# Optimization experiments

Measured on AMD Instinct MI355X. Metric: run time of the kernel, lower is better.

The kernel has to match this reference:

```python
import jax, jax.numpy as jnp
import numpy as np

COMMITMENT_COST = 0.25
ENTROPY_WEIGHT = 0.1
EPS = 1e-10


def setup_inputs() -> dict:
    key = jax.random.key(0)
    k1, k2 = jax.random.split(key)
    B, L, D, K = 8, 4096, 256, 4096
    z = jax.random.normal(k1, (B, L, D), dtype=jnp.float32)
    # torch init: uniform(-1/K, 1/K)
    codebook_weight = jax.random.uniform(k2, (K, D), dtype=jnp.float32,
                                         minval=-1.0 / K, maxval=1.0 / K)
    return {"z": z, "codebook_weight": codebook_weight}


def reference(z, codebook_weight):
    B, L, D = z.shape
    z_flat = z.reshape(-1, D)                       # [N, D]
    # squared euclidean distances: [N, K]
    d2 = (jnp.sum(z_flat ** 2, axis=1, keepdims=True)
          + jnp.sum(codebook_weight ** 2, axis=1)
          - 2.0 * z_flat @ codebook_weight.T)
    indices = jnp.argmin(d2, axis=1)                # [N]
    z_q_flat = codebook_weight[indices]             # gather [N, D]
    z_q = z_q_flat.reshape(B, L, D)

    codebook_loss = jnp.mean((z_q - jax.lax.stop_gradient(z)) ** 2)
    commitment_loss = jnp.mean((jax.lax.stop_gradient(z_q) - z) ** 2)

    probs = jax.nn.softmax(-d2, axis=1)             # [N, K]
    avg_probs = probs.mean(axis=0)                  # [K]
    entropy = -jnp.sum(avg_probs * jnp.log(avg_probs + EPS))
    entropy_loss = -entropy

    codebook_commitment_loss = codebook_loss + COMMITMENT_COST * commitment_loss
    scaled_entropy_loss = ENTROPY_WEIGHT * entropy_loss
    vq_loss = codebook_commitment_loss + scaled_entropy_loss

    # straight-through estimator
    z_q_ste = z + jax.lax.stop_gradient(z_q - z)
    indices_out = indices.reshape(B, L)
    return (z_q_ste, indices_out, vq_loss, codebook_commitment_loss, scaled_entropy_loss)
```

## Files before the change

### kernel.cpp

```cpp
#include <hip/hip_runtime.h>
#include <stdint.h>

#define NROWS 32768
#define KC 4096
#define DIM 256
#define BM 128
#define NWV 8
#define TPS 64
#define CAP 40
#define KAPPA 0.99960f
#define K2L2E 2.88539008f
#define L2E 1.44269504f

#define OUT_IDX (NROWS * DIM)
#define OUT_SCAL (OUT_IDX + NROWS)

#define WS_CNORM 0
#define WS_ZNORM 16384
#define WS_LOSS  147456
#define WS_AVGP8 147712
#define WS_FRAG  278784

typedef __bf16 bf8 __attribute__((ext_vector_type(8)));
typedef float f16v __attribute__((ext_vector_type(16)));

#define GLOAD_LDS(g, l) \
  __builtin_amdgcn_global_load_lds( \
      (const __attribute__((address_space(1))) void*)(g), \
      (__attribute__((address_space(3))) void*)(l), 16, 0, 0)

__device__ __forceinline__ unsigned ford(float f) {
  unsigned u = __float_as_uint(f);
  return (u & 0x80000000u) ? ~u : (u | 0x80000000u);
}

__device__ __forceinline__ float np_rownorm256(const float* __restrict__ p) {
  float h[2];
  #pragma unroll
  for (int half = 0; half < 2; ++half) {
    const float* b = p + half * 128;
    float r[8];
    #pragma unroll
    for (int j = 0; j < 8; ++j) { float v = b[j]; r[j] = __fmul_rn(v, v); }
    for (int i = 8; i < 128; i += 8) {
      #pragma unroll
      for (int j = 0; j < 8; ++j) {
        float v = b[i + j];
        r[j] = __fadd_rn(r[j], __fmul_rn(v, v));
      }
    }
    h[half] = __fadd_rn(
        __fadd_rn(__fadd_rn(r[0], r[1]), __fadd_rn(r[2], r[3])),
        __fadd_rn(__fadd_rn(r[4], r[5]), __fadd_rn(r[6], r[7])));
  }
  return __fadd_rn(h[0], h[1]);
}

__global__ void k_norms(const float* __restrict__ cbw, const float* __restrict__ z,
                        float* __restrict__ cnorm, float* __restrict__ znorm) {
  int r = blockIdx.x * 256 + threadIdx.x;
  if (r < KC) cnorm[r] = np_rownorm256(cbw + (size_t)r * DIM);
  else {
    int q = r - KC;
    if (q < NROWS) znorm[q] = np_rownorm256(z + (size_t)q * DIM);
  }
}

__global__ void k_frag(const float* __restrict__ cbw, __bf16* __restrict__ frag) {
  int idx = blockIdx.x * 256 + threadIdx.x;
  int c = idx >> 5, u = idx & 31;
  int ds = u >> 1, half = u & 1;
  int ct = c >> 5, m = c & 31;
  int lane = half * 32 + m;
  const float* src = cbw + (size_t)c * DIM + ds * 16 + half * 8;
  float4 a = *(const float4*)src;
  float4 b = *(const float4*)(src + 4);
  bf8 h;
  h[0] = (__bf16)a.x; h[1] = (__bf16)a.y; h[2] = (__bf16)a.z; h[3] = (__bf16)a.w;
  h[4] = (__bf16)b.x; h[5] = (__bf16)b.y; h[6] = (__bf16)b.z; h[7] = (__bf16)b.w;
  *(bf8*)(frag + ((size_t)(ct * 16 + ds) * 64 + lane) * 8) = h;
}

__device__ __forceinline__ float exact_d2(const float* __restrict__ zr,
                                          const float* __restrict__ cr,
                                          float rn, float cn) {
  float mm = 0.f;
  for (int d = 0; d < DIM; d += 4) {
    float4 zv = *(const float4*)(zr + d);
    float4 cv = *(const float4*)(cr + d);
    mm = __builtin_fmaf(zv.x, cv.x, mm);
    mm = __builtin_fmaf(zv.y, cv.y, mm);
    mm = __builtin_fmaf(zv.z, cv.z, mm);
    mm = __builtin_fmaf(zv.w, cv.w, mm);
  }
  return __fsub_rn(__fadd_rn(rn, cn), __fmul_rn(2.f, mm));
}

#define BLD(bs, c) (*(const bf8*)((bs) + (c) * 512 + lane * 8))

#define AQ_ALL(OP) OP(0) OP(1) OP(2) OP(3) OP(4) OP(5) OP(6) OP(7) \
                   OP(8) OP(9) OP(10) OP(11) OP(12) OP(13) OP(14) OP(15)
#define AQ_DECL(i) const bf8 aq##i = \
  *(const bf8*)&Aimg[((size_t)(wr * 16 + (i)) * 64 + lane) * 8];

#define MF(A, B) acc = __builtin_amdgcn_mfma_f32_32x32x16_bf16((A), (B), acc, 0, 0, 0);
#define CONSUME_H0(bs) { MF(aq0, BLD(bs,0)) MF(aq1, BLD(bs,1)) MF(aq2, BLD(bs,2)) \
  MF(aq3, BLD(bs,3)) MF(aq4, BLD(bs,4)) MF(aq5, BLD(bs,5)) MF(aq6, BLD(bs,6)) \
  MF(aq7, BLD(bs,7)) }
#define CONSUME_H1(bs) { MF(aq8, BLD(bs,0)) MF(aq9, BLD(bs,1)) MF(aq10, BLD(bs,2)) \
  MF(aq11, BLD(bs,3)) MF(aq12, BLD(bs,4)) MF(aq13, BLD(bs,5)) MF(aq14, BLD(bs,6)) \
  MF(aq15, BLD(bs,7)) }

__global__ __launch_bounds__(512, 2) void k_main(
    const float* __restrict__ z, const float* __restrict__ cbw,
    const float* __restrict__ cnorm, const float* __restrict__ znorm,
    const __bf16* __restrict__ frag, float* __restrict__ out,
    float* __restrict__ avgp8, double* __restrict__ losssum) {
  __shared__ __attribute__((aligned(16))) __bf16 Aimg[4 * 16 * 64 * 8];
  __shared__ __attribute__((aligned(16))) __bf16 Bst[2][2][4096];
  __shared__ float cnormL[KC];
  __shared__ int cand[BM][CAP];
  __shared__ int ccount[BM];
  __shared__ unsigned rowmaxU[BM];
  __shared__ unsigned long long rowkey[BM];
  __shared__ float esumL[BM], invR[BM], lred[512];
  __shared__ int idxr[BM];

  const int t = threadIdx.x;
  const int lane = t & 63, wv = t >> 6;
  const int ln31 = lane & 31, lh = lane >> 5;
  const int wr = wv & 3, wc = wv >> 2;
  const int row0 = blockIdx.x * BM;
  const int ctbase = wc * TPS;

  if (t < BM) {
    ccount[t] = 0; rowmaxU[t] = 0u; rowkey[t] = ~0ULL; esumL[t] = 0.f;
  }

  #pragma unroll
  for (int i = 0; i < 8; ++i) cnormL[t + 512 * i] = cnorm[t + 512 * i];

  #pragma unroll
  for (int i = 0; i < 8; ++i) {
    int idx = i * 512 + t;
    int l = idx & 63, ds = (idx >> 6) & 15, rt = idx >> 10;
    int row = rt * 32 + (l & 31), d0 = ds * 16 + (l >> 5) * 8;
    const float* src = z + (size_t)(row0 + row) * DIM + d0;
    float4 a = *(const float4*)src;
    float4 b = *(const float4*)(src + 4);
    bf8 h;
    h[0] = (__bf16)a.x; h[1] = (__bf16)a.y; h[2] = (__bf16)a.z; h[3] = (__bf16)a.w;
    h[4] = (__bf16)b.x; h[5] = (__bf16)b.y; h[6] = (__bf16)b.z; h[7] = (__bf16)b.w;
    *(bf8*)&Aimg[((size_t)((rt * 16 + ds) * 64 + l)) * 8] = h;
  }
  __syncthreads();

  AQ_ALL(AQ_DECL)

  #define STAGE2(ct, h, buf) { \
    const char* g_ = (const char*)frag + (size_t)(ct) * 16384 + (size_t)(h) * 8192 \
                     + wr * 2048 + (size_t)lane * 16; \
    char* l_ = (char*)Bst + (buf) * 16384 + wc * 8192 + wr * 2048; \
    GLOAD_LDS(g_, l_); \
    GLOAD_LDS(g_ + 1024, l_ + 1024); \
  }

  float es[16];
  #pragma unroll
  for (int i = 0; i < 16; ++i) es[i] = 0.f;

  {
    STAGE2(ctbase, 0, 0)
    __syncthreads();
    for (int tt = 0; tt < 65; ++tt) {
      const int ct = ctbase + (tt ? tt - 1 : 0);
      STAGE2(ct, 1, 1)
      f16v acc;
      #pragma unroll
      for (int r = 0; r < 16; ++r) acc[r] = 0.f;
      float cr[16];
      {
        const float4* rmf = (const float4*)(rowmaxU + wr * 32);
        float4 c0 = rmf[lh], c1 = rmf[2 + lh], c2 = rmf[4 + lh], c3 = rmf[6 + lh];
        cr[0]  = c0.x; cr[1]  = c0.y; cr[2]  = c0.z; cr[3]  = c0.w;
        cr[4]  = c1.x; cr[5]  = c1.y; cr[6]  = c1.z; cr[7]  = c1.w;
        cr[8]  = c2.x; cr[9]  = c2.y; cr[10] = c2.z; cr[11] = c2.w;
        cr[12] = c3.x; cr[13] = c3.y; cr[14] = c3.z; cr[15] = c3.w;
      }
      {
        const __bf16* bs = (const __bf16*)((const char*)Bst + 0 * 16384 + wc * 8192);
        CONSUME_H0(bs)
      }
      __syncthreads();
      {
        int ctn = ctbase + ((tt < 64) ? tt : 63);
        STAGE2(ctn, 0, 0)
      }
      {
        const __bf16* bs = (const __bf16*)((const char*)Bst + 1 * 16384 + wc * 8192);
        CONSUME_H1(bs)
      }
      const float cnl = cnormL[ct * 32 + ln31] * L2E;
      if (tt == 0) {
        #pragma unroll
        for (int r = 0; r < 16; ++r) {
          const int row = wr * 32 + (r & 3) + 8 * (r >> 2) + 4 * lh;
          float e = exp2f(__builtin_fmaf(acc[r], K2L2E, -cnl));
          atomicMax(&rowmaxU[row], __float_as_uint(e));
        }
      } else {
        unsigned cond = 0u;
        #pragma unroll
        for (int r = 0; r < 16; ++r) {
          float e = exp2f(__builtin_fmaf(acc[r], K2L2E, -cnl));
          es[r] += e;
          cond |= (e >= cr[r] * KAPPA) ? (1u << r) : 0u;
        }
        if (cond) {
          #pragma unroll
          for (int r = 0; r < 16; ++r) {
            if (cond & (1u << r)) {
              const int row = wr * 32 + (r & 3) + 8 * (r >> 2) + 4 * lh;
              float e = exp2f(__builtin_fmaf(acc[r], K2L2E, -cnl));
              atomicMax(&rowmaxU[row], __float_as_uint(e));
              int slot = atomicAdd(&ccount[row], 1);
              if (slot < CAP) cand[row][slot] = ct * 32 + ln31;
            }
          }
        }
      }
      __syncthreads();
    }
  }

  #pragma unroll
  for (int r = 0; r < 16; ++r) {
    float e = es[r];
    #pragma unroll
    for (int off = 16; off > 0; off >>= 1) e += __shfl_xor(e, off);
    if (ln31 == 0) {
      const int row = wr * 32 + (r & 3) + 8 * (r >> 2) + 4 * lh;
      atomicAdd(&esumL[row], e);
    }
  }
  __syncthreads();
  if (t < BM) invR[t] = 1.0f / esumL[t];
  __syncthreads();

  {
    int r = t & 127, q = t >> 7;
    int cnt = ccount[r];
    const float* zr = z + (size_t)(row0 + r) * DIM;
    float rn = znorm[row0 + r];
    if (cnt <= CAP) {
      for (int s = q; s < cnt; s += 4) {
        int k = cand[r][s];
        float d2 = exact_d2(zr, cbw + (size_t)k * DIM, rn, cnormL[k]);
        atomicMin(&rowkey[r], (((unsigned long long)ford(d2)) << 32) | (unsigned)k);
      }
    } else {
      for (int k = q; k < KC; k += 4) {
        float d2 = exact_d2(zr, cbw + (size_t)k * DIM, rn, cnormL[k]);
        atomicMin(&rowkey[r], (((unsigned long long)ford(d2)) << 32) | (unsigned)k);
      }
    }
  }
  __syncthreads();
  if (t < BM) {
    int idx = (int)(rowkey[t] & 0xFFFFFFFFULL);
    idxr[t] = idx;
    out[OUT_IDX + row0 + t] = (float)idx;
  }
  __syncthreads();

  float lacc = 0.f;
  {
    const int col = t & 255;
    for (int r = (t >> 8); r < BM; r += 2) {
      int idx = idxr[r];
      float zq = cbw[(size_t)idx * DIM + col];
      float zv = z[(size_t)(row0 + r) * DIM + col];
      float df = __fsub_rn(zq, zv);
      out[(size_t)(row0 + r) * DIM + col] = __fadd_rn(zv, df);
      lacc += df * df;
    }
  }
  lred[t] = lacc;
  __syncthreads();
  #pragma unroll
  for (int s = 256; s > 0; s >>= 1) {
    if (t < s) lred[t] += lred[t + s];
    __syncthreads();
  }
  if (t == 0) atomicAdd(losssum, (double)lred[0]);

  float ir[16];
  #pragma unroll
  for (int r = 0; r < 16; ++r)
    ir[r] = invR[wr * 32 + (r & 3) + 8 * (r >> 2) + 4 * lh];
  __syncthreads();

  {
    float* shadow = avgp8 + (size_t)(blockIdx.x & 7) * KC;
    STAGE2(ctbase, 0, 0)
    __syncthreads();
    for (int tt = 0; tt < 64; ++tt) {
      const int ct = ctbase + tt;
      STAGE2(ct, 1, 1)
      f16v acc;
      #pragma unroll
      for (int r = 0; r < 16; ++r) acc[r] = 0.f;
      {
        const __bf16* bs = (const __bf16*)((const char*)Bst + 0 * 16384 + wc * 8192);
        CONSUME_H0(bs)
      }
      __syncthreads();
      {
        int ctn = ctbase + ((tt < 63) ? tt + 1 : 63);
        STAGE2(ctn, 0, 0)
      }
      {
        const __bf16* bs = (const __bf16*)((const char*)Bst + 1 * 16384 + wc * 8192);
        CONSUME_H1(bs)
      }
      const float cnl = cnormL[ct * 32 + ln31] * L2E;
      float s2 = 0.f;
      #pragma unroll
      for (int r = 0; r < 16; ++r) {
        float e = exp2f(__builtin_fmaf(acc[r], K2L2E, -cnl));
        s2 = __builtin_fmaf(e, ir[r], s2);
      }
      s2 += __shfl_xor(s2, 32);
      if (lh == 0) atomicAdd(&shadow[ct * 32 + ln31], s2);
      __syncthreads();
    }
  }
}

__global__ void k_final(const float* __restrict__ avgp8,
                        const double* __restrict__ losssum,
                        float* __restrict__ out) {
  const int t = threadIdx.x;
  double part = 0.0;
  for (int k = t; k < KC; k += 256) {
    float a4 = 0.f;
    #pragma unroll
    for (int s = 0; s < 8; ++s) a4 += avgp8[s * KC + k];
    double a = (double)a4 / (double)NROWS;
    part += a * log(a + 1e-10);
  }
  __shared__ double sd[256];
  sd[t] = part;
  __syncthreads();
  for (int s = 128; s > 0; s >>= 1) {
    if (t < s) sd[t] += sd[t + s];
    __syncthreads();
  }
  if (t == 0) {
    double H = -sd[0];
    double mse = losssum[0] / (double)((size_t)NROWS * DIM);
    double ccl = 1.25 * mse;
    double sel = -0.1 * H;
    out[OUT_SCAL + 0] = (float)(ccl + sel);
    out[OUT_SCAL + 1] = (float)ccl;
    out[OUT_SCAL + 2] = (float)sel;
  }
}

extern "C" void kernel_launch(void* const* d_in, const int* in_sizes, int n_in,
                              void* d_out, int out_size, void* d_ws, size_t ws_size,
                              hipStream_t stream) {
  const float* z = (const float*)d_in[0];
  const float* cbw = (const float*)d_in[1];
  float* out = (float*)d_out;
  char* ws = (char*)d_ws;
  float* cnorm = (float*)(ws + WS_CNORM);
  float* znorm = (float*)(ws + WS_ZNORM);
  double* losssum = (double*)(ws + WS_LOSS);
  float* avgp8 = (float*)(ws + WS_AVGP8);
  __bf16* frag = (__bf16*)(ws + WS_FRAG);

  hipMemsetAsync(ws + WS_LOSS, 0, 8, stream);
  hipMemsetAsync(ws + WS_AVGP8, 0, 8 * KC * 4, stream);
  k_norms<<<(KC + NROWS) / 256, 256, 0, stream>>>(cbw, z, cnorm, znorm);
  k_frag<<<(KC * 32) / 256, 256, 0, stream>>>(cbw, frag);
  k_main<<<NROWS / BM, 512, 0, stream>>>(z, cbw, cnorm, znorm, frag, out,
                                         avgp8, losssum);
  k_final<<<1, 256, 0, stream>>>(avgp8, losssum, out);
}
```

Measured before the change: 454.2 us.

## Shrink row block to 64 and alias A image with B staging in LDS

```diff
diff --git a/kernel.cpp b/kernel.cpp
--- a/kernel.cpp
+++ b/kernel.cpp
@@ -4,8 +4,8 @@
 #define NROWS 32768
 #define KC 4096
 #define DIM 256
-#define BM 128
-#define NWV 8
+#define BM 64
+#define NWV 4
 #define TPS 64
 #define CAP 40
 #define KAPPA 0.99960f
@@ -101,7 +101,7 @@
 #define AQ_ALL(OP) OP(0) OP(1) OP(2) OP(3) OP(4) OP(5) OP(6) OP(7) \
                    OP(8) OP(9) OP(10) OP(11) OP(12) OP(13) OP(14) OP(15)
 #define AQ_DECL(i) const bf8 aq##i = \
-  *(const bf8*)&Aimg[((size_t)(wr * 16 + (i)) * 64 + lane) * 8];
+  *(const bf8*)&U[((size_t)(wr * 16 + (i)) * 64 + lane) * 8];
 
 #define MF(A, B) acc = __builtin_amdgcn_mfma_f32_32x32x16_bf16((A), (B), acc, 0, 0, 0);
 #define CONSUME_H0(bs) { MF(aq0, BLD(bs,0)) MF(aq1, BLD(bs,1)) MF(aq2, BLD(bs,2)) \
@@ -111,25 +111,23 @@
   MF(aq11, BLD(bs,3)) MF(aq12, BLD(bs,4)) MF(aq13, BLD(bs,5)) MF(aq14, BLD(bs,6)) \
   MF(aq15, BLD(bs,7)) }
 
-__global__ __launch_bounds__(512, 2) void k_main(
+__global__ __launch_bounds__(256, 2) void k_main(
     const float* __restrict__ z, const float* __restrict__ cbw,
     const float* __restrict__ cnorm, const float* __restrict__ znorm,
     const __bf16* __restrict__ frag, float* __restrict__ out,
     float* __restrict__ avgp8, double* __restrict__ losssum) {
-  __shared__ __attribute__((aligned(16))) __bf16 Aimg[4 * 16 * 64 * 8];
-  __shared__ __attribute__((aligned(16))) __bf16 Bst[2][2][4096];
-  __shared__ float cnormL[KC];
+  __shared__ __attribute__((aligned(16))) __bf16 U[16384];
   __shared__ int cand[BM][CAP];
   __shared__ int ccount[BM];
   __shared__ unsigned rowmaxU[BM];
   __shared__ unsigned long long rowkey[BM];
-  __shared__ float esumL[BM], invR[BM], lred[512];
+  __shared__ float esumL[BM], invR[BM], lred[256];
   __shared__ int idxr[BM];
 
   const int t = threadIdx.x;
   const int lane = t & 63, wv = t >> 6;
   const int ln31 = lane & 31, lh = lane >> 5;
-  const int wr = wv & 3, wc = wv >> 2;
+  const int wr = wv >> 1, wc = wv & 1;
   const int row0 = blockIdx.x * BM;
   const int ctbase = wc * TPS;
 
@@ -138,11 +136,8 @@
   }
 
   #pragma unroll
-  for (int i = 0; i < 8; ++i) cnormL[t + 512 * i] = cnorm[t + 512 * i];
-
-  #pragma unroll
   for (int i = 0; i < 8; ++i) {
-    int idx = i * 512 + t;
+    int idx = i * 256 + t;
     int l = idx & 63, ds = (idx >> 6) & 15, rt = idx >> 10;
     int row = rt * 32 + (l & 31), d0 = ds * 16 + (l >> 5) * 8;
     const float* src = z + (size_t)(row0 + row) * DIM + d0;
@@ -151,56 +146,45 @@
     bf8 h;
     h[0] = (__bf16)a.x; h[1] = (__bf16)a.y; h[2] = (__bf16)a.z; h[3] = (__bf16)a.w;
     h[4] = (__bf16)b.x; h[5] = (__bf16)b.y; h[6] = (__bf16)b.z; h[7] = (__bf16)b.w;
-    *(bf8*)&Aimg[((size_t)((rt * 16 + ds) * 64 + l)) * 8] = h;
+    *(bf8*)&U[((size_t)((rt * 16 + ds) * 64 + l)) * 8] = h;
   }
   __syncthreads();
 
   AQ_ALL(AQ_DECL)
-
-  #define STAGE2(ct, h, buf) { \
+  __syncthreads();
+
+  #define STAGEH(ct, h, buf) { \
     const char* g_ = (const char*)frag + (size_t)(ct) * 16384 + (size_t)(h) * 8192 \
-                     + wr * 2048 + (size_t)lane * 16; \
-    char* l_ = (char*)Bst + (buf) * 16384 + wc * 8192 + wr * 2048; \
+                     + wr * 4096 + (size_t)lane * 16; \
+    char* l_ = (char*)U + (buf) * 16384 + wc * 8192 + wr * 4096; \
     GLOAD_LDS(g_, l_); \
     GLOAD_LDS(g_ + 1024, l_ + 1024); \
-  }
+    GLOAD_LDS(g_ + 2048, l_ + 2048); \
+    GLOAD_LDS(g_ + 3072, l_ + 3072); \
+  }
+  #define BSP(buf) ((const __bf16*)((const char*)U + (buf) * 16384 + wc * 8192))
 
   float es[16];
   #pragma unroll
   for (int i = 0; i < 16; ++i) es[i] = 0.f;
 
   {
-    STAGE2(ctbase, 0, 0)
+    STAGEH(ctbase, 0, 0)
     __syncthreads();
     for (int tt = 0; tt < 65; ++tt) {
       const int ct = ctbase + (tt ? tt - 1 : 0);
-      STAGE2(ct, 1, 1)
+      STAGEH(ct, 1, 1)
       f16v acc;
       #pragma unroll
       for (int r = 0; r < 16; ++r) acc[r] = 0.f;
-      float cr[16];
-      {
-        const float4* rmf = (const float4*)(rowmaxU + wr * 32);
-        float4 c0 = rmf[lh], c1 = rmf[2 + lh], c2 = rmf[4 + lh], c3 = rmf[6 + lh];
-        cr[0]  = c0.x; cr[1]  = c0.y; cr[2]  = c0.z; cr[3]  = c0.w;
-        cr[4]  = c1.x; cr[5]  = c1.y; cr[6]  = c1.z; cr[7]  = c1.w;
-        cr[8]  = c2.x; cr[9]  = c2.y; cr[10] = c2.z; cr[11] = c2.w;
-        cr[12] = c3.x; cr[13] = c3.y; cr[14] = c3.z; cr[15] = c3.w;
-      }
-      {
-        const __bf16* bs = (const __bf16*)((const char*)Bst + 0 * 16384 + wc * 8192);
-        CONSUME_H0(bs)
-      }
+      CONSUME_H0(BSP(0))
       __syncthreads();
       {
         int ctn = ctbase + ((tt < 64) ? tt : 63);
-        STAGE2(ctn, 0, 0)
-      }
-      {
-        const __bf16* bs = (const __bf16*)((const char*)Bst + 1 * 16384 + wc * 8192);
-        CONSUME_H1(bs)
-      }
-      const float cnl = cnormL[ct * 32 + ln31] * L2E;
+        STAGEH(ctn, 0, 0)
+      }
+      CONSUME_H1(BSP(1))
+      const float cnl = cnorm[ct * 32 + ln31] * L2E;
       if (tt == 0) {
         #pragma unroll
         for (int r = 0; r < 16; ++r) {
@@ -209,6 +193,15 @@
           atomicMax(&rowmaxU[row], __float_as_uint(e));
         }
       } else {
+        float cr[16];
+        {
+          const float4* rmf = (const float4*)(rowmaxU + wr * 32);
+          float4 c0 = rmf[lh], c1 = rmf[2 + lh], c2 = rmf[4 + lh], c3 = rmf[6 + lh];
+          cr[0]  = c0.x; cr[1]  = c0.y; cr[2]  = c0.z; cr[3]  = c0.w;
+          cr[4]  = c1.x; cr[5]  = c1.y; cr[6]  = c1.z; cr[7]  = c1.w;
+          cr[8]  = c2.x; cr[9]  = c2.y; cr[10] = c2.z; cr[11] = c2.w;
+          cr[12] = c3.x; cr[13] = c3.y; cr[14] = c3.z; cr[15] = c3.w;
+        }
         unsigned cond = 0u;
         #pragma unroll
         for (int r = 0; r < 16; ++r) {
@@ -248,19 +241,19 @@
   __syncthreads();
 
   {
-    int r = t & 127, q = t >> 7;
+    int r = t & 63, q = t >> 6;
     int cnt = ccount[r];
     const float* zr = z + (size_t)(row0 + r) * DIM;
     float rn = znorm[row0 + r];
     if (cnt <= CAP) {
       for (int s = q; s < cnt; s += 4) {
         int k = cand[r][s];
-        float d2 = exact_d2(zr, cbw + (size_t)k * DIM, rn, cnormL[k]);
+        float d2 = exact_d2(zr, cbw + (size_t)k * DIM, rn, cnorm[k]);
         atomicMin(&rowkey[r], (((unsigned long long)ford(d2)) << 32) | (unsigned)k);
       }
     } else {
       for (int k = q; k < KC; k += 4) {
-        float d2 = exact_d2(zr, cbw + (size_t)k * DIM, rn, cnormL[k]);
+        float d2 = exact_d2(zr, cbw + (size_t)k * DIM, rn, cnorm[k]);
         atomicMin(&rowkey[r], (((unsigned long long)ford(d2)) << 32) | (unsigned)k);
       }
     }
@@ -274,21 +267,18 @@
   __syncthreads();
 
   float lacc = 0.f;
-  {
-    const int col = t & 255;
-    for (int r = (t >> 8); r < BM; r += 2) {
-      int idx = idxr[r];
-      float zq = cbw[(size_t)idx * DIM + col];
-      float zv = z[(size_t)(row0 + r) * DIM + col];
-      float df = __fsub_rn(zq, zv);
-      out[(size_t)(row0 + r) * DIM + col] = __fadd_rn(zv, df);
-      lacc += df * df;
-    }
+  for (int r = 0; r < BM; ++r) {
+    int idx = idxr[r];
+    float zq = cbw[(size_t)idx * DIM + t];
+    float zv = z[(size_t)(row0 + r) * DIM + t];
+    float df = __fsub_rn(zq, zv);
+    out[(size_t)(row0 + r) * DIM + t] = __fadd_rn(zv, df);
+    lacc += df * df;
   }
   lred[t] = lacc;
   __syncthreads();
   #pragma unroll
-  for (int s = 256; s > 0; s >>= 1) {
+  for (int s = 128; s > 0; s >>= 1) {
     if (t < s) lred[t] += lred[t + s];
     __syncthreads();
   }
@@ -302,28 +292,22 @@
 
   {
     float* shadow = avgp8 + (size_t)(blockIdx.x & 7) * KC;
-    STAGE2(ctbase, 0, 0)
+    STAGEH(ctbase, 0, 0)
     __syncthreads();
     for (int tt = 0; tt < 64; ++tt) {
       const int ct = ctbase + tt;
-      STAGE2(ct, 1, 1)
+      STAGEH(ct, 1, 1)
       f16v acc;
       #pragma unroll
       for (int r = 0; r < 16; ++r) acc[r] = 0.f;
-      {
-        const __bf16* bs = (const __bf16*)((const char*)Bst + 0 * 16384 + wc * 8192);
-        CONSUME_H0(bs)
-      }
+      CONSUME_H0(BSP(0))
       __syncthreads();
       {
         int ctn = ctbase + ((tt < 63) ? tt + 1 : 63);
-        STAGE2(ctn, 0, 0)
-      }
-      {
-        const __bf16* bs = (const __bf16*)((const char*)Bst + 1 * 16384 + wc * 8192);
-        CONSUME_H1(bs)
-      }
-      const float cnl = cnormL[ct * 32 + ln31] * L2E;
+        STAGEH(ctn, 0, 0)
+      }
+      CONSUME_H1(BSP(1))
+      const float cnl = cnorm[ct * 32 + ln31] * L2E;
       float s2 = 0.f;
       #pragma unroll
       for (int r = 0; r < 16; ++r) {
@@ -384,7 +368,7 @@
   hipMemsetAsync(ws + WS_AVGP8, 0, 8 * KC * 4, stream);
   k_norms<<<(KC + NROWS) / 256, 256, 0, stream>>>(cbw, z, cnorm, znorm);
   k_frag<<<(KC * 32) / 256, 256, 0, stream>>>(cbw, frag);
-  k_main<<<NROWS / BM, 512, 0, stream>>>(z, cbw, cnorm, znorm, frag, out,
+  k_main<<<NROWS / BM, 256, 0, stream>>>(z, cbw, cnorm, znorm, frag, out,
                                          avgp8, losssum);
   k_final<<<1, 256, 0, stream>>>(avgp8, losssum, out);
 }
```

New measurement: 439.3 us. 3.3% less time.

## Retile waves to 64x32 output tiles with A fragments streamed from LDS

Applied to the files above, without the earlier changes.

```diff
diff --git a/kernel.cpp b/kernel.cpp
--- a/kernel.cpp
+++ b/kernel.cpp
@@ -6,7 +6,8 @@
 #define DIM 256
 #define BM 128
 #define NWV 8
-#define TPS 64
+#define NST 4
+#define TPS 32
 #define CAP 40
 #define KAPPA 0.99960f
 #define K2L2E 2.88539008f
@@ -96,29 +97,13 @@
   return __fsub_rn(__fadd_rn(rn, cn), __fmul_rn(2.f, mm));
 }
 
-#define BLD(bs, c) (*(const bf8*)((bs) + (c) * 512 + lane * 8))
-
-#define AQ_ALL(OP) OP(0) OP(1) OP(2) OP(3) OP(4) OP(5) OP(6) OP(7) \
-                   OP(8) OP(9) OP(10) OP(11) OP(12) OP(13) OP(14) OP(15)
-#define AQ_DECL(i) const bf8 aq##i = \
-  *(const bf8*)&Aimg[((size_t)(wr * 16 + (i)) * 64 + lane) * 8];
-
-#define MF(A, B) acc = __builtin_amdgcn_mfma_f32_32x32x16_bf16((A), (B), acc, 0, 0, 0);
-#define CONSUME_H0(bs) { MF(aq0, BLD(bs,0)) MF(aq1, BLD(bs,1)) MF(aq2, BLD(bs,2)) \
-  MF(aq3, BLD(bs,3)) MF(aq4, BLD(bs,4)) MF(aq5, BLD(bs,5)) MF(aq6, BLD(bs,6)) \
-  MF(aq7, BLD(bs,7)) }
-#define CONSUME_H1(bs) { MF(aq8, BLD(bs,0)) MF(aq9, BLD(bs,1)) MF(aq10, BLD(bs,2)) \
-  MF(aq11, BLD(bs,3)) MF(aq12, BLD(bs,4)) MF(aq13, BLD(bs,5)) MF(aq14, BLD(bs,6)) \
-  MF(aq15, BLD(bs,7)) }
-
 __global__ __launch_bounds__(512, 2) void k_main(
     const float* __restrict__ z, const float* __restrict__ cbw,
     const float* __restrict__ cnorm, const float* __restrict__ znorm,
     const __bf16* __restrict__ frag, float* __restrict__ out,
     float* __restrict__ avgp8, double* __restrict__ losssum) {
   __shared__ __attribute__((aligned(16))) __bf16 Aimg[4 * 16 * 64 * 8];
-  __shared__ __attribute__((aligned(16))) __bf16 Bst[2][2][4096];
-  __shared__ float cnormL[KC];
+  __shared__ __attribute__((aligned(16))) __bf16 Bst[2][NST][4096];
   __shared__ int cand[BM][CAP];
   __shared__ int ccount[BM];
   __shared__ unsigned rowmaxU[BM];
@@ -129,16 +114,14 @@
   const int t = threadIdx.x;
   const int lane = t & 63, wv = t >> 6;
   const int ln31 = lane & 31, lh = lane >> 5;
-  const int wr = wv & 3, wc = wv >> 2;
+  const int g = wv >> 2, sid = wv & 3;
+  const int g2 = g * 2;
   const int row0 = blockIdx.x * BM;
-  const int ctbase = wc * TPS;
+  const int ctbase = sid * TPS;
 
   if (t < BM) {
     ccount[t] = 0; rowmaxU[t] = 0u; rowkey[t] = ~0ULL; esumL[t] = 0.f;
   }
-
-  #pragma unroll
-  for (int i = 0; i < 8; ++i) cnormL[t + 512 * i] = cnorm[t + 512 * i];
 
   #pragma unroll
   for (int i = 0; i < 8; ++i) {
@@ -155,79 +138,97 @@
   }
   __syncthreads();
 
-  AQ_ALL(AQ_DECL)
-
-  #define STAGE2(ct, h, buf) { \
+  #define STG(ct, h, b) { \
     const char* g_ = (const char*)frag + (size_t)(ct) * 16384 + (size_t)(h) * 8192 \
-                     + wr * 2048 + (size_t)lane * 16; \
-    char* l_ = (char*)Bst + (buf) * 16384 + wc * 8192 + wr * 2048; \
+                     + g * 4096 + (size_t)lane * 16; \
+    char* l_ = (char*)Bst + ((b) * NST + sid) * 8192 + g * 4096; \
     GLOAD_LDS(g_, l_); \
     GLOAD_LDS(g_ + 1024, l_ + 1024); \
-  }
-
-  float es[16];
-  #pragma unroll
-  for (int i = 0; i < 16; ++i) es[i] = 0.f;
+    GLOAD_LDS(g_ + 2048, l_ + 2048); \
+    GLOAD_LDS(g_ + 3072, l_ + 3072); \
+  }
+
+  #define CONS(b, h) { \
+    const __bf16* bs_ = (const __bf16*)((const char*)Bst + ((b) * NST + sid) * 8192); \
+    _Pragma("unroll") \
+    for (int c_ = 0; c_ < 8; ++c_) { \
+      bf8 Bf = *(const bf8*)(bs_ + c_ * 512 + lane * 8); \
+      bf8 A0 = *(const bf8*)&Aimg[((size_t)(((g2    ) * 16 + (h) * 8 + c_) * 64 + lane)) * 8]; \
+      bf8 A1 = *(const bf8*)&Aimg[((size_t)(((g2 + 1) * 16 + (h) * 8 + c_) * 64 + lane)) * 8]; \
+      accA = __builtin_amdgcn_mfma_f32_32x32x16_bf16(A0, Bf, accA, 0, 0, 0); \
+      accB = __builtin_amdgcn_mfma_f32_32x32x16_bf16(A1, Bf, accB, 0, 0, 0); \
+    } \
+  }
+
+  #define CRLOAD(cr, ROFF) { \
+    const float4* rmf_ = (const float4*)(rowmaxU + (ROFF)); \
+    float4 c0 = rmf_[lh], c1 = rmf_[2 + lh], c2 = rmf_[4 + lh], c3 = rmf_[6 + lh]; \
+    cr[0]  = c0.x; cr[1]  = c0.y; cr[2]  = c0.z; cr[3]  = c0.w; \
+    cr[4]  = c1.x; cr[5]  = c1.y; cr[6]  = c1.z; cr[7]  = c1.w; \
+    cr[8]  = c2.x; cr[9]  = c2.y; cr[10] = c2.z; cr[11] = c2.w; \
+    cr[12] = c3.x; cr[13] = c3.y; cr[14] = c3.z; cr[15] = c3.w; \
+  }
+
+  #define EPI1(ACC, ES, ROFF) { \
+    float cr[16]; \
+    CRLOAD(cr, ROFF) \
+    unsigned cond = 0u; \
+    _Pragma("unroll") \
+    for (int r = 0; r < 16; ++r) { \
+      float e = exp2f(__builtin_fmaf(ACC[r], K2L2E, -cnl)); \
+      ES[r] += e;                        \
+      cond |= (e >= cr[r] * KAPPA) ? (1u << r) : 0u; \
+    } \
+    if (cond) {    \
+      _Pragma("unroll") \
+      for (int r = 0; r < 16; ++r) { \
+        if (cond & (1u << r)) { \
+          const int row = (ROFF) + (r & 3) + 8 * (r >> 2) + 4 * lh; \
+          float e = exp2f(__builtin_fmaf(ACC[r], K2L2E, -cnl)); \
+          atomicMax(&rowmaxU[row], __float_as_uint(e)); \
+          int slot = atomicAdd(&ccount[row], 1); \
+          if (slot < CAP) cand[row][slot] = ct * 32 + ln31; \
+        } \
+      } \
+    } \
+  }
+
+  #define PRIME(ACC, ROFF) { \
+    _Pragma("unroll") \
+    for (int r = 0; r < 16; ++r) { \
+      const int row = (ROFF) + (r & 3) + 8 * (r >> 2) + 4 * lh; \
+      float e = exp2f(__builtin_fmaf(ACC[r], K2L2E, -cnl)); \
+      atomicMax(&rowmaxU[row], __float_as_uint(e));   \
+    } \
+  }
+
+  float esA[16], esB[16];
+  #pragma unroll
+  for (int i = 0; i < 16; ++i) { esA[i] = 0.f; esB[i] = 0.f; }
 
   {
-    STAGE2(ctbase, 0, 0)
+    STG(ctbase, 0, 0)
     __syncthreads();
-    for (int tt = 0; tt < 65; ++tt) {
+    for (int tt = 0; tt <= TPS; ++tt) {
       const int ct = ctbase + (tt ? tt - 1 : 0);
-      STAGE2(ct, 1, 1)
-      f16v acc;
+      STG(ct, 1, 1)
+      f16v accA, accB;
       #pragma unroll
-      for (int r = 0; r < 16; ++r) acc[r] = 0.f;
-      float cr[16];
-      {
-        const float4* rmf = (const float4*)(rowmaxU + wr * 32);
-        float4 c0 = rmf[lh], c1 = rmf[2 + lh], c2 = rmf[4 + lh], c3 = rmf[6 + lh];
-        cr[0]  = c0.x; cr[1]  = c0.y; cr[2]  = c0.z; cr[3]  = c0.w;
-        cr[4]  = c1.x; cr[5]  = c1.y; cr[6]  = c1.z; cr[7]  = c1.w;
-        cr[8]  = c2.x; cr[9]  = c2.y; cr[10] = c2.z; cr[11] = c2.w;
-        cr[12] = c3.x; cr[13] = c3.y; cr[14] = c3.z; cr[15] = c3.w;
-      }
-      {
-        const __bf16* bs = (const __bf16*)((const char*)Bst + 0 * 16384 + wc * 8192);
-        CONSUME_H0(bs)
-      }
+      for (int r = 0; r < 16; ++r) { accA[r] = 0.f; accB[r] = 0.f; }
+      CONS(0, 0)
       __syncthreads();
       {
-        int ctn = ctbase + ((tt < 64) ? tt : 63);
-        STAGE2(ctn, 0, 0)
-      }
-      {
-        const __bf16* bs = (const __bf16*)((const char*)Bst + 1 * 16384 + wc * 8192);
-        CONSUME_H1(bs)
-      }
-      const float cnl = cnormL[ct * 32 + ln31] * L2E;
+        int ctn = ctbase + ((tt < TPS) ? tt : TPS - 1);
+        STG(ctn, 0, 0)
+      }
+      CONS(1, 1)
+      const float cnl = cnorm[ct * 32 + ln31] * L2E;
       if (tt == 0) {
-        #pragma unroll
-        for (int r = 0; r < 16; ++r) {
-          const int row = wr * 32 + (r & 3) + 8 * (r >> 2) + 4 * lh;
-          float e = exp2f(__builtin_fmaf(acc[r], K2L2E, -cnl));
-          atomicMax(&rowmaxU[row], __float_as_uint(e));
-        }
+        PRIME(accA, g * 64)
+        PRIME(accB, g * 64 + 32)
       } else {
-        unsigned cond = 0u;
-        #pragma unroll
-        for (int r = 0; r < 16; ++r) {
-          float e = exp2f(__builtin_fmaf(acc[r], K2L2E, -cnl));
-          es[r] += e;
-          cond |= (e >= cr[r] * KAPPA) ? (1u << r) : 0u;
-        }
-        if (cond) {
-          #pragma unroll
-          for (int r = 0; r < 16; ++r) {
-            if (cond & (1u << r)) {
-              const int row = wr * 32 + (r & 3) + 8 * (r >> 2) + 4 * lh;
-              float e = exp2f(__builtin_fmaf(acc[r], K2L2E, -cnl));
-              atomicMax(&rowmaxU[row], __float_as_uint(e));
-              int slot = atomicAdd(&ccount[row], 1);
-              if (slot < CAP) cand[row][slot] = ct * 32 + ln31;
-            }
-          }
-        }
+        EPI1(accA, esA, g * 64)
+        EPI1(accB, esB, g * 64 + 32)
       }
       __syncthreads();
     }
@@ -235,12 +236,16 @@
 
   #pragma unroll
   for (int r = 0; r < 16; ++r) {
-    float e = es[r];
+    float eA = esA[r], eB = esB[r];
     #pragma unroll
-    for (int off = 16; off > 0; off >>= 1) e += __shfl_xor(e, off);
+    for (int off = 16; off > 0; off >>= 1) {
+      eA += __shfl_xor(eA, off);
+      eB += __shfl_xor(eB, off);
+    }
     if (ln31 == 0) {
-      const int row = wr * 32 + (r & 3) + 8 * (r >> 2) + 4 * lh;
-      atomicAdd(&esumL[row], e);
+      const int crow = (r & 3) + 8 * (r >> 2) + 4 * lh;
+      atomicAdd(&esumL[g * 64 + crow], eA);
+      atomicAdd(&esumL[g * 64 + 32 + crow], eB);
     }
   }
   __syncthreads();
@@ -255,12 +260,12 @@
     if (cnt <= CAP) {
       for (int s = q; s < cnt; s += 4) {
         int k = cand[r][s];
-        float d2 = exact_d2(zr, cbw + (size_t)k * DIM, rn, cnormL[k]);
+        float d2 = exact_d2(zr, cbw + (size_t)k * DIM, rn, cnorm[k]);
         atomicMin(&rowkey[r], (((unsigned long long)ford(d2)) << 32) | (unsigned)k);
       }
     } else {
       for (int k = q; k < KC; k += 4) {
-        float d2 = exact_d2(zr, cbw + (size_t)k * DIM, rn, cnormL[k]);
+        float d2 = exact_d2(zr, cbw + (size_t)k * DIM, rn, cnorm[k]);
         atomicMin(&rowkey[r], (((unsigned long long)ford(d2)) << 32) | (unsigned)k);
       }
     }
@@ -294,41 +299,40 @@
   }
   if (t == 0) atomicAdd(losssum, (double)lred[0]);
 
-  float ir[16];
-  #pragma unroll
-  for (int r = 0; r < 16; ++r)
-    ir[r] = invR[wr * 32 + (r & 3) + 8 * (r >> 2) + 4 * lh];
+  float irA[16], irB[16];
+  #pragma unroll
+  for (int r = 0; r < 16; ++r) {
+    const int crow = (r & 3) + 8 * (r >> 2) + 4 * lh;
+    irA[r] = invR[g * 64 + crow];
+    irB[r] = invR[g * 64 + 32 + crow];
+  }
   __syncthreads();
 
   {
     float* shadow = avgp8 + (size_t)(blockIdx.x & 7) * KC;
-    STAGE2(ctbase, 0, 0)
+    STG(ctbase, 0, 0)
     __syncthreads();
-    for (int tt = 0; tt < 64; ++tt) {
+    for (int tt = 0; tt < TPS; ++tt) {
       const int ct = ctbase + tt;
-      STAGE2(ct, 1, 1)
-      f16v acc;
+      STG(ct, 1, 1)
+      f16v accA, accB;
       #pragma unroll
-      for (int r = 0; r < 16; ++r) acc[r] = 0.f;
-      {
-        const __bf16* bs = (const __bf16*)((const char*)Bst + 0 * 16384 + wc * 8192);
-        CONSUME_H0(bs)
-      }
+      for (int r = 0; r < 16; ++r) { accA[r] = 0.f; accB[r] = 0.f; }
+      CONS(0, 0)
       __syncthreads();
       {
-        int ctn = ctbase + ((tt < 63) ? tt + 1 : 63);
-        STAGE2(ctn, 0, 0)
-      }
-      {
-        const __bf16* bs = (const __bf16*)((const char*)Bst + 1 * 16384 + wc * 8192);
-        CONSUME_H1(bs)
-      }
-      const float cnl = cnormL[ct * 32 + ln31] * L2E;
+        int ctn = ctbase + ((tt < TPS - 1) ? tt + 1 : TPS - 1);
+        STG(ctn, 0, 0)
+      }
+      CONS(1, 1)
+      const float cnl = cnorm[ct * 32 + ln31] * L2E;
       float s2 = 0.f;
       #pragma unroll
       for (int r = 0; r < 16; ++r) {
-        float e = exp2f(__builtin_fmaf(acc[r], K2L2E, -cnl));
-        s2 = __builtin_fmaf(e, ir[r], s2);
+        float eA = exp2f(__builtin_fmaf(accA[r], K2L2E, -cnl));
+        s2 = __builtin_fmaf(eA, irA[r], s2);
+        float eB = exp2f(__builtin_fmaf(accB[r], K2L2E, -cnl));
+        s2 = __builtin_fmaf(eB, irB[r], s2);
       }
       s2 += __shfl_xor(s2, 32);
       if (lh == 0) atomicAdd(&shadow[ct * 32 + ln31], s2);
```

Measured after the change: 449.1 us. No clear change (-1.1%).
